# Kernel optimization log

Measured on AMD Instinct MI355X. Metric: run time of the kernel, lower is better.

Reference implementation:

```python
import jax, jax.numpy as jnp
import numpy as np

B, BITS, HID = 4096, 64, 512
EPS = 1e-5
TEMPERATURE = 1.0  # buffer default


def _w(k, shape):
    return jax.random.normal(k, shape, jnp.float32) * 0.02


def setup_inputs() -> dict:
    key = jax.random.key(0)
    ks = jax.random.split(key, 8)
    return {
        "a_bits": jax.random.uniform(ks[0], (B, BITS), jnp.float32),
        "shift_bits": jax.random.uniform(ks[1], (B, BITS), jnp.float32),
        # shift_decoder params
        "W1": _w(ks[2], (HID, BITS)), "b1": jnp.zeros((HID,), jnp.float32),
        "g1": jnp.ones((HID,), jnp.float32), "be1": jnp.zeros((HID,), jnp.float32),
        "W2": _w(ks[3], (HID, HID)), "b2": jnp.zeros((HID,), jnp.float32),
        "g2": jnp.ones((HID,), jnp.float32), "be2": jnp.zeros((HID,), jnp.float32),
        "W3": _w(ks[4], (BITS, HID)), "b3": jnp.zeros((BITS,), jnp.float32),
        # index_net params (input dim = 2*BITS)
        "Wi1": _w(ks[5], (HID, 2 * BITS)), "bi1": jnp.zeros((HID,), jnp.float32),
        "Wi2": _w(ks[6], (HID, HID)), "bi2": jnp.zeros((HID,), jnp.float32),
        "Wi3": _w(ks[7], (BITS, HID)), "bi3": jnp.zeros((BITS,), jnp.float32),
    }


def _layernorm(x, g, b):
    m = jnp.mean(x, axis=-1, keepdims=True)
    v = jnp.mean(jnp.square(x - m), axis=-1, keepdims=True)
    return (x - m) * jax.lax.rsqrt(v + EPS) * g + b


def reference(a_bits, shift_bits, W1, b1, g1, be1, W2, b2, g2, be2, W3, b3,
              Wi1, bi1, Wi2, bi2, Wi3, bi3):
    # shift decoder: Linear -> LN -> ReLU -> Linear -> LN -> ReLU -> Linear
    h = jax.nn.relu(_layernorm(shift_bits @ W1.T + b1, g1, be1))
    h = jax.nn.relu(_layernorm(h @ W2.T + b2, g2, be2))
    shift_logits = h @ W3.T + b3                        # [B, BITS]
    shift_soft = jax.nn.softmax(shift_logits / TEMPERATURE, axis=-1)

    # index_net, vectorized over the output-position loop.
    # combined = [one_hot(i), shift_soft]; the one-hot part of the first Linear
    # just selects column i of Wi1[:, :BITS], so we add it as a [BITS, HID] bias.
    pos_part = Wi1[:, :BITS].T                          # [BITS, HID]
    shift_part = shift_soft @ Wi1[:, BITS:].T           # [B, HID]
    h1 = jax.nn.relu(pos_part[None, :, :] + shift_part[:, None, :] + bi1)  # [B, BITS, HID]
    h2 = jax.nn.relu(jnp.einsum('bph,kh->bpk', h1, Wi2) + bi2)             # [B, BITS, HID]
    idx_logits = jnp.einsum('bph,kh->bpk', h2, Wi3) + bi3                  # [B, BITS, BITS]
    idx_soft = jax.nn.softmax(idx_logits / TEMPERATURE, axis=-1)

    # softmax-weighted gather-sum over a_bits
    return jnp.einsum('bpj,bj->bp', idx_soft, a_bits)   # [B, BITS]
```

## Files before the change

kernel.cpp:

```cpp
#include <hip/hip_runtime.h>
#include <hip/hip_bf16.h>
#include <math.h>

#define B_N 4096
#define BITSN 64
#define HID 512
#define EPSV 1e-5f
#define BT 16

typedef unsigned short ushort_t;
typedef __attribute__((ext_vector_type(8))) short bf16x8;
typedef __attribute__((ext_vector_type(4))) float f32x4;
typedef __attribute__((ext_vector_type(16))) float f32x16;

__device__ __forceinline__ ushort_t f2bf(float f) {
  unsigned u = __float_as_uint(f);
  u += 0x7FFF + ((u >> 16) & 1);
  return (ushort_t)(u >> 16);
}

__device__ __forceinline__ unsigned pack2bf(float lo, float hi) {
  union { __hip_bfloat162 h; unsigned u; } cv;
  cv.h = __float22bfloat162_rn(make_float2(lo, hi));
  return cv.u;
}

__device__ __forceinline__ float bf2f(short v) {
  return __uint_as_float(((unsigned)(unsigned short)v) << 16);
}

__global__ __launch_bounds__(256) void prep_kernel(
    const float* __restrict__ Wi2, const float* __restrict__ Wi3,
    const float* __restrict__ Wi1, const float* __restrict__ W1,
    const float* __restrict__ W2, const float* __restrict__ W3,
    ushort_t* __restrict__ Wi1posTb, ushort_t* __restrict__ W1b,
    ushort_t* __restrict__ W2b, ushort_t* __restrict__ W3b,
    ushort_t* __restrict__ Wi1sb, ushort_t* __restrict__ Wi2f32,
    ushort_t* __restrict__ Wi3g) {
  int idx = blockIdx.x * 256 + threadIdx.x;
  if (idx < 512 * 512) {
    W2b[idx] = f2bf(W2[idx]);
    int j = idx & 7, lane = (idx >> 3) & 63;
    int ct = (idx >> 9) & 15, ks = idx >> 13;
    int c = ct * 32 + (lane & 31);
    int k = ks * 16 + (lane >> 5) * 8 + j;
    Wi2f32[idx] = f2bf(Wi2[c * 512 + k]);
  }
  if (idx < 64 * 512) {
    W3b[idx] = f2bf(W3[idx]);
    int p = idx >> 9, i = idx & 511;
    Wi1posTb[idx] = f2bf(Wi1[i * 128 + p]);
    int e = idx & 7, lane = (idx >> 3) & 63;
    int jt = (idx >> 9) & 1, h = (idx >> 10) & 1;
    int mc = (idx >> 11) & 1, w = idx >> 12;
    int jr = jt * 32 + (lane & 31);
    int c = w * 64 + mc * 32 + 16 * h + 4 * (lane >> 5) + (e & 3) + 8 * (e >> 2);
    Wi3g[idx] = f2bf(Wi3[jr * 512 + c]);
  }
  if (idx < 512 * 64) {
    W1b[idx] = f2bf(W1[idx]);
    int j = idx >> 6, k = idx & 63;
    Wi1sb[idx] = f2bf(Wi1[j * 128 + 64 + k]);
  }
}

__global__ __launch_bounds__(256) void shift2_kernel(
    const float* __restrict__ shift_bits,
    const ushort_t* __restrict__ W1b, const float* __restrict__ b1,
    const float* __restrict__ g1, const float* __restrict__ be1,
    const ushort_t* __restrict__ W2b, const float* __restrict__ b2,
    const float* __restrict__ g2, const float* __restrict__ be2,
    const ushort_t* __restrict__ W3b, const float* __restrict__ b3,
    const ushort_t* __restrict__ Wi1sb, const float* __restrict__ bi1,
    float* __restrict__ sp) {
  __shared__ __align__(16) ushort_t hA[BT * 512];
  __shared__ __align__(16) char reg2[32 * 1024];
  __shared__ float b1s[512], g1s[512], be1s[512];
  __shared__ float b2s[512], g2s[512], be2s[512], bi1s[512];
  __shared__ float red[4][BT][2];
  __shared__ float b3s[64];

  ushort_t* sbt = (ushort_t*)reg2;
  ushort_t* Bs  = (ushort_t*)reg2;
  ushort_t* h2  = (ushort_t*)reg2;
  float (*lg32)[68] = (float(*)[68])(reg2 + 16 * 1024);
  ushort_t* sb2 = (ushort_t*)(reg2 + 16 * 1024 + 16 * 68 * 4);

  int b0 = blockIdx.x * BT;
  int t = threadIdx.x, w = t >> 6, l = t & 63, lg = l >> 4, l15 = l & 15;

  b1s[t] = b1[t];  b1s[t + 256] = b1[t + 256];
  g1s[t] = g1[t];  g1s[t + 256] = g1[t + 256];
  be1s[t] = be1[t]; be1s[t + 256] = be1[t + 256];
  b2s[t] = b2[t];  b2s[t + 256] = b2[t + 256];
  g2s[t] = g2[t];  g2s[t + 256] = g2[t + 256];
  be2s[t] = be2[t]; be2s[t + 256] = be2[t + 256];
  bi1s[t] = bi1[t]; bi1s[t + 256] = bi1[t + 256];
  if (t < 64) b3s[t] = b3[t];
  if (t < 128) {
    int row = t >> 3, g = t & 7;
    const float* src = shift_bits + (size_t)(b0 + row) * 64 + g * 8;
    uint4 pk;
    pk.x = (unsigned)f2bf(src[0]) | ((unsigned)f2bf(src[1]) << 16);
    pk.y = (unsigned)f2bf(src[2]) | ((unsigned)f2bf(src[3]) << 16);
    pk.z = (unsigned)f2bf(src[4]) | ((unsigned)f2bf(src[5]) << 16);
    pk.w = (unsigned)f2bf(src[6]) | ((unsigned)f2bf(src[7]) << 16);
    *(uint4*)((char*)sbt + ((row * 128 + g * 16) ^ ((row & 7) << 4))) = pk;
  }
  __syncthreads();

  f32x4 acc[8];
#pragma unroll
  for (int nt = 0; nt < 8; ++nt) acc[nt] = (f32x4){0.f, 0.f, 0.f, 0.f};
#pragma unroll
  for (int ks = 0; ks < 2; ++ks) {
    bf16x8 af = *(const bf16x8*)((char*)sbt + ((l15 * 128 + ks * 64 + lg * 16) ^ ((l15 & 7) << 4)));
#pragma unroll
    for (int nt = 0; nt < 8; ++nt) {
      int c = w * 128 + nt * 16 + l15;
      bf16x8 bfr = *(const bf16x8*)(W1b + (size_t)c * 64 + ks * 32 + lg * 8);
      acc[nt] = __builtin_amdgcn_mfma_f32_16x16x32_bf16(af, bfr, acc[nt], 0, 0, 0);
    }
  }
  {
    float s[4] = {0.f, 0.f, 0.f, 0.f}, q[4] = {0.f, 0.f, 0.f, 0.f};
#pragma unroll
    for (int nt = 0; nt < 8; ++nt) {
      int c = w * 128 + nt * 16 + l15;
      float bb = b1s[c];
#pragma unroll
      for (int r = 0; r < 4; ++r) {
        float x = acc[nt][r] + bb;
        acc[nt][r] = x;
        s[r] += x; q[r] += x * x;
      }
    }
#pragma unroll
    for (int m = 8; m >= 1; m >>= 1)
#pragma unroll
      for (int r = 0; r < 4; ++r) { s[r] += __shfl_xor(s[r], m); q[r] += __shfl_xor(q[r], m); }
    if (l15 == 0)
#pragma unroll
      for (int r = 0; r < 4; ++r) { red[w][4 * lg + r][0] = s[r]; red[w][4 * lg + r][1] = q[r]; }
    __syncthreads();
    float mean[4], rs[4];
#pragma unroll
    for (int r = 0; r < 4; ++r) {
      int p = 4 * lg + r;
      float S = red[0][p][0] + red[1][p][0] + red[2][p][0] + red[3][p][0];
      float Q = red[0][p][1] + red[1][p][1] + red[2][p][1] + red[3][p][1];
      mean[r] = S * (1.0f / 512.0f);
      float var = Q * (1.0f / 512.0f) - mean[r] * mean[r];
      rs[r] = rsqrtf(var + EPSV);
    }
#pragma unroll
    for (int nt = 0; nt < 8; ++nt) {
      int c = w * 128 + nt * 16 + l15;
      float gg = g1s[c], bb = be1s[c];
#pragma unroll
      for (int r = 0; r < 4; ++r) {
        int p = 4 * lg + r;
        float v = (acc[nt][r] - mean[r]) * rs[r] * gg + bb;
        v = v > 0.f ? v : 0.f;
        *(ushort_t*)((char*)hA + ((p * 1024 + c * 2) ^ ((p & 7) << 4))) = f2bf(v);
      }
    }
  }
  __syncthreads();

#pragma unroll
  for (int nt = 0; nt < 8; ++nt) acc[nt] = (f32x4){0.f, 0.f, 0.f, 0.f};
  for (int step = 0; step < 16; ++step) {
    int i0 = step * 32;
#pragma unroll
    for (int qq = 0; qq < 8; ++qq) {
      int g = qq * 256 + t;
      int c = g >> 2, xg = g & 3;
      int ic = xg ^ ((c >> 1) & 3);
      ((uint4*)Bs)[g] = *(const uint4*)(W2b + (size_t)c * 512 + i0 + ic * 8);
    }
    __syncthreads();
    bf16x8 af = *(const bf16x8*)((char*)hA + ((l15 * 1024 + step * 64 + lg * 16) ^ ((l15 & 7) << 4)));
#pragma unroll
    for (int nt = 0; nt < 8; ++nt) {
      int c = w * 128 + nt * 16 + l15;
      bf16x8 bfr = ((const bf16x8*)Bs)[c * 4 + (lg ^ ((c >> 1) & 3))];
      acc[nt] = __builtin_amdgcn_mfma_f32_16x16x32_bf16(af, bfr, acc[nt], 0, 0, 0);
    }
    __syncthreads();
  }
  {
    float s[4] = {0.f, 0.f, 0.f, 0.f}, q[4] = {0.f, 0.f, 0.f, 0.f};
#pragma unroll
    for (int nt = 0; nt < 8; ++nt) {
      int c = w * 128 + nt * 16 + l15;
      float bb = b2s[c];
#pragma unroll
      for (int r = 0; r < 4; ++r) {
        float x = acc[nt][r] + bb;
        acc[nt][r] = x;
        s[r] += x; q[r] += x * x;
      }
    }
#pragma unroll
    for (int m = 8; m >= 1; m >>= 1)
#pragma unroll
      for (int r = 0; r < 4; ++r) { s[r] += __shfl_xor(s[r], m); q[r] += __shfl_xor(q[r], m); }
    if (l15 == 0)
#pragma unroll
      for (int r = 0; r < 4; ++r) { red[w][4 * lg + r][0] = s[r]; red[w][4 * lg + r][1] = q[r]; }
    __syncthreads();
    float mean[4], rs[4];
#pragma unroll
    for (int r = 0; r < 4; ++r) {
      int p = 4 * lg + r;
      float S = red[0][p][0] + red[1][p][0] + red[2][p][0] + red[3][p][0];
      float Q = red[0][p][1] + red[1][p][1] + red[2][p][1] + red[3][p][1];
      mean[r] = S * (1.0f / 512.0f);
      float var = Q * (1.0f / 512.0f) - mean[r] * mean[r];
      rs[r] = rsqrtf(var + EPSV);
    }
#pragma unroll
    for (int nt = 0; nt < 8; ++nt) {
      int c = w * 128 + nt * 16 + l15;
      float gg = g2s[c], bb = be2s[c];
#pragma unroll
      for (int r = 0; r < 4; ++r) {
        int p = 4 * lg + r;
        float v = (acc[nt][r] - mean[r]) * rs[r] * gg + bb;
        v = v > 0.f ? v : 0.f;
        *(ushort_t*)((char*)h2 + ((p * 1024 + c * 2) ^ ((p & 7) << 4))) = f2bf(v);
      }
    }
  }
  __syncthreads();

  {
    f32x4 a3 = (f32x4){0.f, 0.f, 0.f, 0.f};
#pragma unroll
    for (int ks = 0; ks < 16; ++ks) {
      bf16x8 af = *(const bf16x8*)((char*)h2 + ((l15 * 1024 + ks * 64 + lg * 16) ^ ((l15 & 7) << 4)));
      bf16x8 bfr = *(const bf16x8*)(W3b + (size_t)(w * 16 + l15) * 512 + ks * 32 + lg * 8);
      a3 = __builtin_amdgcn_mfma_f32_16x16x32_bf16(af, bfr, a3, 0, 0, 0);
    }
    int c = w * 16 + l15;
    float bb = b3s[c];
#pragma unroll
    for (int r = 0; r < 4; ++r) lg32[4 * lg + r][c] = a3[r] + bb;
  }
  __syncthreads();

  {
    int r = t >> 4, j = t & 15;
    float v[4];
    float m = -1e30f;
#pragma unroll
    for (int mq = 0; mq < 4; ++mq) { v[mq] = lg32[r][mq * 16 + j]; m = fmaxf(m, v[mq]); }
#pragma unroll
    for (int mk = 8; mk >= 1; mk >>= 1) m = fmaxf(m, __shfl_xor(m, mk));
    float ssum = 0.f;
#pragma unroll
    for (int mq = 0; mq < 4; ++mq) { v[mq] = expf(v[mq] - m); ssum += v[mq]; }
#pragma unroll
    for (int mk = 8; mk >= 1; mk >>= 1) ssum += __shfl_xor(ssum, mk);
    float inv = 1.f / ssum;
#pragma unroll
    for (int mq = 0; mq < 4; ++mq) {
      int c = mq * 16 + j;
      *(ushort_t*)((char*)sb2 + ((r * 128 + c * 2) ^ ((r & 7) << 4))) = f2bf(v[mq] * inv);
    }
  }
  __syncthreads();

  {
    f32x4 a4[8];
#pragma unroll
    for (int nt = 0; nt < 8; ++nt) a4[nt] = (f32x4){0.f, 0.f, 0.f, 0.f};
#pragma unroll
    for (int ks = 0; ks < 2; ++ks) {
      bf16x8 af = *(const bf16x8*)((char*)sb2 + ((l15 * 128 + ks * 64 + lg * 16) ^ ((l15 & 7) << 4)));
#pragma unroll
      for (int nt = 0; nt < 8; ++nt) {
        int c = w * 128 + nt * 16 + l15;
        bf16x8 bfr = *(const bf16x8*)(Wi1sb + (size_t)c * 64 + ks * 32 + lg * 8);
        a4[nt] = __builtin_amdgcn_mfma_f32_16x16x32_bf16(af, bfr, a4[nt], 0, 0, 0);
      }
    }
#pragma unroll
    for (int nt = 0; nt < 8; ++nt) {
      int c = w * 128 + nt * 16 + l15;
      float bb = bi1s[c];
#pragma unroll
      for (int r = 0; r < 4; ++r)
        sp[(size_t)(b0 + 4 * lg + r) * 512 + c] = a4[nt][r] + bb;
    }
  }
}

__global__ __launch_bounds__(512, 4) void big8_kernel(
    const float* __restrict__ a_bits, const float* __restrict__ sp,
    const ushort_t* __restrict__ posTb,
    const ushort_t* __restrict__ Wi2f32, const ushort_t* __restrict__ Wi3g,
    const float* __restrict__ bi2, const float* __restrict__ bi3,
    float* __restrict__ out) {
  __shared__ __align__(16) ushort_t h1s[64 * 512];
  __shared__ float bi2s[512];
  __shared__ float ab[64];
  __shared__ float bi3s[64];

  int b = blockIdx.x, t = threadIdx.x;
  int w = t >> 6, l = t & 63;
  int l31 = l & 31, hi = l >> 5;

  bi2s[t] = bi2[t];
  if (t < 64) { ab[t] = a_bits[b * 64 + t]; bi3s[t] = bi3[t]; }

  {
    const float* sprow = sp + (size_t)b * 512 + l * 8;
    float4 s0 = *(const float4*)(sprow);
    float4 s1 = *(const float4*)(sprow + 4);
#pragma unroll
    for (int g = 0; g < 8; ++g) {
      int p = g * 8 + w;
      bf16x8 pr = *(const bf16x8*)(posTb + (size_t)p * 512 + l * 8);
      float v0 = fmaxf(s0.x + bf2f(pr[0]), 0.f), v1 = fmaxf(s0.y + bf2f(pr[1]), 0.f);
      float v2 = fmaxf(s0.z + bf2f(pr[2]), 0.f), v3 = fmaxf(s0.w + bf2f(pr[3]), 0.f);
      float v4 = fmaxf(s1.x + bf2f(pr[4]), 0.f), v5 = fmaxf(s1.y + bf2f(pr[5]), 0.f);
      float v6 = fmaxf(s1.z + bf2f(pr[6]), 0.f), v7 = fmaxf(s1.w + bf2f(pr[7]), 0.f);
      uint4 pk;
      pk.x = pack2bf(v0, v1); pk.y = pack2bf(v2, v3);
      pk.z = pack2bf(v4, v5); pk.w = pack2bf(v6, v7);
      *(uint4*)((char*)h1s + ((p * 1024 + l * 16) ^ ((p & 15) << 4))) = pk;
    }
  }
  __syncthreads();

  f32x16 acc[2][2];
#pragma unroll
  for (int mc = 0; mc < 2; ++mc)
#pragma unroll
    for (int np = 0; np < 2; ++np)
#pragma unroll
      for (int r = 0; r < 16; ++r) acc[mc][np][r] = 0.f;

  {
    const bf16x8* bbase = (const bf16x8*)Wi2f32 + ((size_t)(2 * w) * 64 + l);
    bf16x8 wf[4][2];
#pragma unroll
    for (int d = 0; d < 4; ++d) {
      wf[d][0] = bbase[(size_t)d * 1024];
      wf[d][1] = bbase[(size_t)d * 1024 + 64];
    }
    for (int kb = 0; kb < 8; ++kb) {
#pragma unroll
      for (int d = 0; d < 4; ++d) {
        int ks = kb * 4 + d;
        bf16x8 w0 = wf[d][0], w1 = wf[d][1];
        if (kb < 7) {
          wf[d][0] = bbase[(size_t)(ks + 4) * 1024];
          wf[d][1] = bbase[(size_t)(ks + 4) * 1024 + 64];
        }
        int row0 = l31, row1 = 32 + l31;
        bf16x8 h0 = *(const bf16x8*)((char*)h1s + ((row0 * 1024 + ks * 32 + hi * 16) ^ ((row0 & 15) << 4)));
        bf16x8 h1v = *(const bf16x8*)((char*)h1s + ((row1 * 1024 + ks * 32 + hi * 16) ^ ((row1 & 15) << 4)));
        acc[0][0] = __builtin_amdgcn_mfma_f32_32x32x16_bf16(w0, h0, acc[0][0], 0, 0, 0);
        acc[0][1] = __builtin_amdgcn_mfma_f32_32x32x16_bf16(w0, h1v, acc[0][1], 0, 0, 0);
        acc[1][0] = __builtin_amdgcn_mfma_f32_32x32x16_bf16(w1, h0, acc[1][0], 0, 0, 0);
        acc[1][1] = __builtin_amdgcn_mfma_f32_32x32x16_bf16(w1, h1v, acc[1][1], 0, 0, 0);
      }
    }
  }

  bf16x8 pkf[2][2][2];
#pragma unroll
  for (int mc = 0; mc < 2; ++mc) {
    float bia[16];
#pragma unroll
    for (int rq = 0; rq < 4; ++rq) {
      int c0 = w * 64 + mc * 32 + 8 * rq + 4 * hi;
      float4 bi4 = *(const float4*)(bi2s + c0);
      bia[4 * rq + 0] = bi4.x; bia[4 * rq + 1] = bi4.y;
      bia[4 * rq + 2] = bi4.z; bia[4 * rq + 3] = bi4.w;
    }
#pragma unroll
    for (int np = 0; np < 2; ++np) {
      float hv[16];
#pragma unroll
      for (int r = 0; r < 16; ++r) hv[r] = fmaxf(acc[mc][np][r] + bia[r], 0.f);
#pragma unroll
      for (int h = 0; h < 2; ++h) {
        unsigned d0 = pack2bf(hv[8 * h + 0], hv[8 * h + 1]);
        unsigned d1 = pack2bf(hv[8 * h + 2], hv[8 * h + 3]);
        unsigned d2 = pack2bf(hv[8 * h + 4], hv[8 * h + 5]);
        unsigned d3 = pack2bf(hv[8 * h + 6], hv[8 * h + 7]);
        union { unsigned u[4]; bf16x8 v; } cv;
        cv.u[0] = d0; cv.u[1] = d1; cv.u[2] = d2; cv.u[3] = d3;
        pkf[np][mc][h] = cv.v;
      }
    }
  }
  __syncthreads();

  f32x16 l00, l01, l10, l11;
#pragma unroll
  for (int r = 0; r < 16; ++r) { l00[r] = 0.f; l01[r] = 0.f; l10[r] = 0.f; l11[r] = 0.f; }
  {
    const bf16x8* gbase = (const bf16x8*)Wi3g + ((size_t)w * 8 * 64 + l);
#pragma unroll
    for (int mc = 0; mc < 2; ++mc) {
#pragma unroll
      for (int h = 0; h < 2; ++h) {
        bf16x8 g0 = gbase[((mc * 2 + h) * 2 + 0) * 64];
        bf16x8 g1 = gbase[((mc * 2 + h) * 2 + 1) * 64];
        l00 = __builtin_amdgcn_mfma_f32_32x32x16_bf16(pkf[0][mc][h], g0, l00, 0, 0, 0);
        l01 = __builtin_amdgcn_mfma_f32_32x32x16_bf16(pkf[0][mc][h], g1, l01, 0, 0, 0);
        l10 = __builtin_amdgcn_mfma_f32_32x32x16_bf16(pkf[1][mc][h], g0, l10, 0, 0, 0);
        l11 = __builtin_amdgcn_mfma_f32_32x32x16_bf16(pkf[1][mc][h], g1, l11, 0, 0, 0);
      }
    }
  }

  float* Lg = (float*)h1s;
  if (w < 4) {
    float* Lq = Lg + w * 4096;
#pragma unroll
    for (int rq = 0; rq < 4; ++rq) {
      int rb = 8 * rq + 4 * hi;
      int cA = l31, cB = 32 + l31;
      *(float4*)(Lq + cA * 64 + (rb ^ ((cA & 7) << 3))) =
          make_float4(l00[4*rq], l00[4*rq+1], l00[4*rq+2], l00[4*rq+3]);
      *(float4*)(Lq + cB * 64 + (rb ^ ((cB & 7) << 3))) =
          make_float4(l01[4*rq], l01[4*rq+1], l01[4*rq+2], l01[4*rq+3]);
      *(float4*)(Lq + cA * 64 + ((rb + 32) ^ ((cA & 7) << 3))) =
          make_float4(l10[4*rq], l10[4*rq+1], l10[4*rq+2], l10[4*rq+3]);
      *(float4*)(Lq + cB * 64 + ((rb + 32) ^ ((cB & 7) << 3))) =
          make_float4(l11[4*rq], l11[4*rq+1], l11[4*rq+2], l11[4*rq+3]);
    }
  }
  __syncthreads();
  if (w >= 4) {
    float* Lq = Lg + (w - 4) * 4096;
#pragma unroll
    for (int rq = 0; rq < 4; ++rq) {
      int rb = 8 * rq + 4 * hi;
      int cA = l31, cB = 32 + l31;
      float* pA0 = Lq + cA * 64 + (rb ^ ((cA & 7) << 3));
      float* pB0 = Lq + cB * 64 + (rb ^ ((cB & 7) << 3));
      float* pA1 = Lq + cA * 64 + ((rb + 32) ^ ((cA & 7) << 3));
      float* pB1 = Lq + cB * 64 + ((rb + 32) ^ ((cB & 7) << 3));
      float4 oA0 = *(float4*)pA0, oB0 = *(float4*)pB0;
      float4 oA1 = *(float4*)pA1, oB1 = *(float4*)pB1;
      oA0.x += l00[4*rq]; oA0.y += l00[4*rq+1]; oA0.z += l00[4*rq+2]; oA0.w += l00[4*rq+3];
      oB0.x += l01[4*rq]; oB0.y += l01[4*rq+1]; oB0.z += l01[4*rq+2]; oB0.w += l01[4*rq+3];
      oA1.x += l10[4*rq]; oA1.y += l10[4*rq+1]; oA1.z += l10[4*rq+2]; oA1.w += l10[4*rq+3];
      oB1.x += l11[4*rq]; oB1.y += l11[4*rq+1]; oB1.z += l11[4*rq+2]; oB1.w += l11[4*rq+3];
      *(float4*)pA0 = oA0; *(float4*)pB0 = oB0;
      *(float4*)pA1 = oA1; *(float4*)pB1 = oB1;
    }
  }
  __syncthreads();

  {
    int p = t >> 3, jo = t & 7;
    float s = 0.f, g = 0.f;
#pragma unroll
    for (int m = 0; m < 8; ++m) {
      int c = jo * 8 + m;
      int off = c * 64 + (p ^ ((c & 7) << 3));
      float lv = bi3s[c] + Lg[off] + Lg[4096 + off] + Lg[8192 + off] + Lg[12288 + off];
      float e = __expf(lv);
      s += e; g += e * ab[c];
    }
#pragma unroll
    for (int mm = 4; mm >= 1; mm >>= 1) { s += __shfl_xor(s, mm); g += __shfl_xor(g, mm); }
    if (jo == 0) out[b * 64 + p] = g / s;
  }
}

extern "C" void kernel_launch(void* const* d_in, const int* in_sizes, int n_in,
                              void* d_out, int out_size, void* d_ws, size_t ws_size,
                              hipStream_t stream) {
  const float* a_bits     = (const float*)d_in[0];
  const float* shift_bits = (const float*)d_in[1];
  const float* W1  = (const float*)d_in[2];
  const float* b1  = (const float*)d_in[3];
  const float* g1  = (const float*)d_in[4];
  const float* be1 = (const float*)d_in[5];
  const float* W2  = (const float*)d_in[6];
  const float* b2  = (const float*)d_in[7];
  const float* g2  = (const float*)d_in[8];
  const float* be2 = (const float*)d_in[9];
  const float* W3  = (const float*)d_in[10];
  const float* b3  = (const float*)d_in[11];
  const float* Wi1 = (const float*)d_in[12];
  const float* bi1 = (const float*)d_in[13];
  const float* Wi2 = (const float*)d_in[14];
  const float* bi2 = (const float*)d_in[15];
  const float* Wi3 = (const float*)d_in[16];
  const float* bi3 = (const float*)d_in[17];
  float* out = (float*)d_out;

  float* sp = (float*)d_ws;
  ushort_t* W2b = (ushort_t*)((char*)d_ws + (size_t)B_N * HID * 4);
  ushort_t* W1b = W2b + 512 * 512;
  ushort_t* W3b = W1b + 512 * 64;
  ushort_t* Wi1sb = W3b + 64 * 512;
  ushort_t* Wi1posTb = Wi1sb + 512 * 64;
  ushort_t* Wi2f32 = Wi1posTb + 64 * 512;
  ushort_t* Wi3g = Wi2f32 + 512 * 512;

  prep_kernel<<<1024, 256, 0, stream>>>(Wi2, Wi3, Wi1, W1, W2, W3,
                                        Wi1posTb, W1b, W2b, W3b, Wi1sb, Wi2f32, Wi3g);
  shift2_kernel<<<B_N / BT, 256, 0, stream>>>(shift_bits, W1b, b1, g1, be1,
                                              W2b, b2, g2, be2, W3b, b3, Wi1sb, bi1, sp);
  big8_kernel<<<B_N, 512, 0, stream>>>(a_bits, sp, Wi1posTb, Wi2f32, Wi3g, bi2, bi3, out);
}
```

Before: 204.3 us.

## Prepack W2 into MFMA fragment order, add setprio, reduce logits in bf16 LDS

W2 is prepacked into MFMA fragment order, so the shift kernel loads B fragments straight from global memory. This drops the staged LDS copy and the two barriers on each K step. In the big kernel, MFMA groups are wrapped in s_setprio to favour matrix issue. The cross-wave logit reduction now has all 8 waves write bf16 partials to LDS at once and sums them in a single pass, replacing two serialized fp32 phases. The bf16 partials reduce precision of the logits before softmax.

```diff
diff --git a/kernel.cpp b/kernel.cpp
--- a/kernel.cpp
+++ b/kernel.cpp
@@ -34,17 +34,25 @@
     const float* __restrict__ Wi1, const float* __restrict__ W1,
     const float* __restrict__ W2, const float* __restrict__ W3,
     ushort_t* __restrict__ Wi1posTb, ushort_t* __restrict__ W1b,
-    ushort_t* __restrict__ W2b, ushort_t* __restrict__ W3b,
+    ushort_t* __restrict__ W2f, ushort_t* __restrict__ W3b,
     ushort_t* __restrict__ Wi1sb, ushort_t* __restrict__ Wi2f32,
     ushort_t* __restrict__ Wi3g) {
   int idx = blockIdx.x * 256 + threadIdx.x;
   if (idx < 512 * 512) {
-    W2b[idx] = f2bf(W2[idx]);
-    int j = idx & 7, lane = (idx >> 3) & 63;
-    int ct = (idx >> 9) & 15, ks = idx >> 13;
-    int c = ct * 32 + (lane & 31);
-    int k = ks * 16 + (lane >> 5) * 8 + j;
-    Wi2f32[idx] = f2bf(Wi2[c * 512 + k]);
+    {
+      int j = idx & 7, lane = (idx >> 3) & 63;
+      int ct = (idx >> 9) & 31, ks = idx >> 14;
+      int c = ct * 16 + (lane & 15);
+      int k = ks * 32 + (lane >> 4) * 8 + j;
+      W2f[idx] = f2bf(W2[c * 512 + k]);
+    }
+    {
+      int j = idx & 7, lane = (idx >> 3) & 63;
+      int ct = (idx >> 9) & 15, ks = idx >> 13;
+      int c = ct * 32 + (lane & 31);
+      int k = ks * 16 + (lane >> 5) * 8 + j;
+      Wi2f32[idx] = f2bf(Wi2[c * 512 + k]);
+    }
   }
   if (idx < 64 * 512) {
     W3b[idx] = f2bf(W3[idx]);
@@ -68,7 +76,7 @@
     const float* __restrict__ shift_bits,
     const ushort_t* __restrict__ W1b, const float* __restrict__ b1,
     const float* __restrict__ g1, const float* __restrict__ be1,
-    const ushort_t* __restrict__ W2b, const float* __restrict__ b2,
+    const ushort_t* __restrict__ W2f, const float* __restrict__ b2,
     const float* __restrict__ g2, const float* __restrict__ be2,
     const ushort_t* __restrict__ W3b, const float* __restrict__ b3,
     const ushort_t* __restrict__ Wi1sb, const float* __restrict__ bi1,
@@ -81,7 +89,6 @@
   __shared__ float b3s[64];
 
   ushort_t* sbt = (ushort_t*)reg2;
-  ushort_t* Bs  = (ushort_t*)reg2;
   ushort_t* h2  = (ushort_t*)reg2;
   float (*lg32)[68] = (float(*)[68])(reg2 + 16 * 1024);
   ushort_t* sb2 = (ushort_t*)(reg2 + 16 * 1024 + 16 * 68 * 4);
@@ -170,25 +177,19 @@
 
 #pragma unroll
   for (int nt = 0; nt < 8; ++nt) acc[nt] = (f32x4){0.f, 0.f, 0.f, 0.f};
-  for (int step = 0; step < 16; ++step) {
-    int i0 = step * 32;
-#pragma unroll
-    for (int qq = 0; qq < 8; ++qq) {
-      int g = qq * 256 + t;
-      int c = g >> 2, xg = g & 3;
-      int ic = xg ^ ((c >> 1) & 3);
-      ((uint4*)Bs)[g] = *(const uint4*)(W2b + (size_t)c * 512 + i0 + ic * 8);
-    }
-    __syncthreads();
-    bf16x8 af = *(const bf16x8*)((char*)hA + ((l15 * 1024 + step * 64 + lg * 16) ^ ((l15 & 7) << 4)));
-#pragma unroll
-    for (int nt = 0; nt < 8; ++nt) {
-      int c = w * 128 + nt * 16 + l15;
-      bf16x8 bfr = ((const bf16x8*)Bs)[c * 4 + (lg ^ ((c >> 1) & 3))];
-      acc[nt] = __builtin_amdgcn_mfma_f32_16x16x32_bf16(af, bfr, acc[nt], 0, 0, 0);
-    }
-    __syncthreads();
-  }
+  {
+    const bf16x8* w2base = (const bf16x8*)W2f + ((size_t)(w * 8) * 64 + l);
+#pragma unroll 2
+    for (int step = 0; step < 16; ++step) {
+      bf16x8 af = *(const bf16x8*)((char*)hA + ((l15 * 1024 + step * 64 + lg * 16) ^ ((l15 & 7) << 4)));
+#pragma unroll
+      for (int nt = 0; nt < 8; ++nt) {
+        bf16x8 bfr = w2base[((size_t)step * 32 + nt) * 64];
+        acc[nt] = __builtin_amdgcn_mfma_f32_16x16x32_bf16(af, bfr, acc[nt], 0, 0, 0);
+      }
+    }
+  }
+  __syncthreads();
   {
     float s[4] = {0.f, 0.f, 0.f, 0.f}, q[4] = {0.f, 0.f, 0.f, 0.f};
 #pragma unroll
@@ -297,7 +298,7 @@
   }
 }
 
-__global__ __launch_bounds__(512, 4) void big8_kernel(
+__global__ __launch_bounds__(512, 4) void big9_kernel(
     const float* __restrict__ a_bits, const float* __restrict__ sp,
     const ushort_t* __restrict__ posTb,
     const ushort_t* __restrict__ Wi2f32, const ushort_t* __restrict__ Wi3g,
@@ -363,10 +364,12 @@
         int row0 = l31, row1 = 32 + l31;
         bf16x8 h0 = *(const bf16x8*)((char*)h1s + ((row0 * 1024 + ks * 32 + hi * 16) ^ ((row0 & 15) << 4)));
         bf16x8 h1v = *(const bf16x8*)((char*)h1s + ((row1 * 1024 + ks * 32 + hi * 16) ^ ((row1 & 15) << 4)));
+        __builtin_amdgcn_s_setprio(1);
         acc[0][0] = __builtin_amdgcn_mfma_f32_32x32x16_bf16(w0, h0, acc[0][0], 0, 0, 0);
         acc[0][1] = __builtin_amdgcn_mfma_f32_32x32x16_bf16(w0, h1v, acc[0][1], 0, 0, 0);
         acc[1][0] = __builtin_amdgcn_mfma_f32_32x32x16_bf16(w1, h0, acc[1][0], 0, 0, 0);
         acc[1][1] = __builtin_amdgcn_mfma_f32_32x32x16_bf16(w1, h1v, acc[1][1], 0, 0, 0);
+        __builtin_amdgcn_s_setprio(0);
       }
     }
   }
@@ -412,63 +415,45 @@
       for (int h = 0; h < 2; ++h) {
         bf16x8 g0 = gbase[((mc * 2 + h) * 2 + 0) * 64];
         bf16x8 g1 = gbase[((mc * 2 + h) * 2 + 1) * 64];
+        __builtin_amdgcn_s_setprio(1);
         l00 = __builtin_amdgcn_mfma_f32_32x32x16_bf16(pkf[0][mc][h], g0, l00, 0, 0, 0);
         l01 = __builtin_amdgcn_mfma_f32_32x32x16_bf16(pkf[0][mc][h], g1, l01, 0, 0, 0);
         l10 = __builtin_amdgcn_mfma_f32_32x32x16_bf16(pkf[1][mc][h], g0, l10, 0, 0, 0);
         l11 = __builtin_amdgcn_mfma_f32_32x32x16_bf16(pkf[1][mc][h], g1, l11, 0, 0, 0);
-      }
-    }
-  }
-
-  float* Lg = (float*)h1s;
-  if (w < 4) {
-    float* Lq = Lg + w * 4096;
-#pragma unroll
-    for (int rq = 0; rq < 4; ++rq) {
-      int rb = 8 * rq + 4 * hi;
-      int cA = l31, cB = 32 + l31;
-      *(float4*)(Lq + cA * 64 + (rb ^ ((cA & 7) << 3))) =
-          make_float4(l00[4*rq], l00[4*rq+1], l00[4*rq+2], l00[4*rq+3]);
-      *(float4*)(Lq + cB * 64 + (rb ^ ((cB & 7) << 3))) =
-          make_float4(l01[4*rq], l01[4*rq+1], l01[4*rq+2], l01[4*rq+3]);
-      *(float4*)(Lq + cA * 64 + ((rb + 32) ^ ((cA & 7) << 3))) =
-          make_float4(l10[4*rq], l10[4*rq+1], l10[4*rq+2], l10[4*rq+3]);
-      *(float4*)(Lq + cB * 64 + ((rb + 32) ^ ((cB & 7) << 3))) =
-          make_float4(l11[4*rq], l11[4*rq+1], l11[4*rq+2], l11[4*rq+3]);
-    }
-  }
-  __syncthreads();
-  if (w >= 4) {
-    float* Lq = Lg + (w - 4) * 4096;
-#pragma unroll
-    for (int rq = 0; rq < 4; ++rq) {
-      int rb = 8 * rq + 4 * hi;
-      int cA = l31, cB = 32 + l31;
-      float* pA0 = Lq + cA * 64 + (rb ^ ((cA & 7) << 3));
-      float* pB0 = Lq + cB * 64 + (rb ^ ((cB & 7) << 3));
-      float* pA1 = Lq + cA * 64 + ((rb + 32) ^ ((cA & 7) << 3));
-      float* pB1 = Lq + cB * 64 + ((rb + 32) ^ ((cB & 7) << 3));
-      float4 oA0 = *(float4*)pA0, oB0 = *(float4*)pB0;
-      float4 oA1 = *(float4*)pA1, oB1 = *(float4*)pB1;
-      oA0.x += l00[4*rq]; oA0.y += l00[4*rq+1]; oA0.z += l00[4*rq+2]; oA0.w += l00[4*rq+3];
-      oB0.x += l01[4*rq]; oB0.y += l01[4*rq+1]; oB0.z += l01[4*rq+2]; oB0.w += l01[4*rq+3];
-      oA1.x += l10[4*rq]; oA1.y += l10[4*rq+1]; oA1.z += l10[4*rq+2]; oA1.w += l10[4*rq+3];
-      oB1.x += l11[4*rq]; oB1.y += l11[4*rq+1]; oB1.z += l11[4*rq+2]; oB1.w += l11[4*rq+3];
-      *(float4*)pA0 = oA0; *(float4*)pB0 = oB0;
-      *(float4*)pA1 = oA1; *(float4*)pB1 = oB1;
+        __builtin_amdgcn_s_setprio(0);
+      }
+    }
+  }
+
+  {
+    ushort_t* Pr = h1s + (size_t)w * 4096;
+#pragma unroll
+    for (int r = 0; r < 16; ++r) {
+      int p0 = (r & 3) + 8 * (r >> 2) + 4 * hi;
+      int p1 = p0 + 32;
+      Pr[p0 * 64 + ((l31)      ^ (8 * (p0 & 7)))] = f2bf(l00[r]);
+      Pr[p0 * 64 + ((32 + l31) ^ (8 * (p0 & 7)))] = f2bf(l01[r]);
+      Pr[p1 * 64 + ((l31)      ^ (8 * (p1 & 7)))] = f2bf(l10[r]);
+      Pr[p1 * 64 + ((32 + l31) ^ (8 * (p1 & 7)))] = f2bf(l11[r]);
     }
   }
   __syncthreads();
 
   {
     int p = t >> 3, jo = t & 7;
+    int off = p * 64 + ((jo ^ (p & 7)) * 8);
+    float sum[8] = {0.f, 0.f, 0.f, 0.f, 0.f, 0.f, 0.f, 0.f};
+#pragma unroll
+    for (int wr = 0; wr < 8; ++wr) {
+      bf16x8 v = *(const bf16x8*)(h1s + wr * 4096 + off);
+#pragma unroll
+      for (int m = 0; m < 8; ++m) sum[m] += bf2f(v[m]);
+    }
     float s = 0.f, g = 0.f;
 #pragma unroll
     for (int m = 0; m < 8; ++m) {
       int c = jo * 8 + m;
-      int off = c * 64 + (p ^ ((c & 7) << 3));
-      float lv = bi3s[c] + Lg[off] + Lg[4096 + off] + Lg[8192 + off] + Lg[12288 + off];
-      float e = __expf(lv);
+      float e = __expf(sum[m] + bi3s[c]);
       s += e; g += e * ab[c];
     }
 #pragma unroll
@@ -501,8 +486,8 @@
   float* out = (float*)d_out;
 
   float* sp = (float*)d_ws;
-  ushort_t* W2b = (ushort_t*)((char*)d_ws + (size_t)B_N * HID * 4);
-  ushort_t* W1b = W2b + 512 * 512;
+  ushort_t* W2f = (ushort_t*)((char*)d_ws + (size_t)B_N * HID * 4);
+  ushort_t* W1b = W2f + 512 * 512;
   ushort_t* W3b = W1b + 512 * 64;
   ushort_t* Wi1sb = W3b + 64 * 512;
   ushort_t* Wi1posTb = Wi1sb + 512 * 64;
@@ -510,8 +495,8 @@
   ushort_t* Wi3g = Wi2f32 + 512 * 512;
 
   prep_kernel<<<1024, 256, 0, stream>>>(Wi2, Wi3, Wi1, W1, W2, W3,
-                                        Wi1posTb, W1b, W2b, W3b, Wi1sb, Wi2f32, Wi3g);
+                                        Wi1posTb, W1b, W2f, W3b, Wi1sb, Wi2f32, Wi3g);
   shift2_kernel<<<B_N / BT, 256, 0, stream>>>(shift_bits, W1b, b1, g1, be1,
-                                              W2b, b2, g2, be2, W3b, b3, Wi1sb, bi1, sp);
-  big8_kernel<<<B_N, 512, 0, stream>>>(a_bits, sp, Wi1posTb, Wi2f32, Wi3g, bi2, bi3, out);
-}
+                                              W2f, b2, g2, be2, W3b, b3, Wi1sb, bi1, sp);
+  big9_kernel<<<B_N, 512, 0, stream>>>(a_bits, sp, Wi1posTb, Wi2f32, Wi3g, bi2, bi3, out);
+}
```

New measurement: 202.2 us. About the same (-1.0%).
